# Kernel tuning notes

Measured on AMD Instinct MI355X. Metric: run time of the kernel, lower is better.

## Reference

```python
import jax, jax.numpy as jnp
import numpy as np

MAX_SEQLEN = 2048  # static max sequence length (flash varlen APIs take this as a host arg)


def setup_inputs() -> dict:
    key = jax.random.key(0)
    k1, k2, k3 = jax.random.split(key, 3)
    T, H, D = 8192, 8, 128
    B = 4
    q = jax.random.normal(k1, (T, H, D), dtype=jnp.float32)
    k = jax.random.normal(k2, (T, H, D), dtype=jnp.float32)
    v = jax.random.normal(k3, (T, H, D), dtype=jnp.float32)
    cu = (jnp.arange(B + 1, dtype=jnp.int32) * (T // B))  # [0,2048,4096,6144,8192]
    return {"q": q, "k": k, "v": v, "cu_seqlens_q": cu, "cu_seqlens_k": cu}


def reference(q, k, v, cu_seqlens_q, cu_seqlens_k):
    """Varlen (ragged) multi-head attention, non-causal (flash_attn varlen default).

    q,k,v: [T, H, D] packed over sequences; cu_seqlens: [B+1] boundaries.
    Gathers each sequence into a padded [B, S, H, D] layout, computes
    per-sequence softmax(q k^T / sqrt(D)) v with padding masked, then
    scatters back to packed [T, H, D].
    """
    T, H, D = q.shape
    B = cu_seqlens_q.shape[0] - 1
    S = MAX_SEQLEN
    scale = 1.0 / jnp.sqrt(jnp.asarray(D, q.dtype))

    pos = jnp.arange(S)
    q_start = cu_seqlens_q[:-1]
    k_start = cu_seqlens_k[:-1]
    q_len = jnp.diff(cu_seqlens_q)  # [B]
    k_len = jnp.diff(cu_seqlens_k)

    q_idx = jnp.clip(q_start[:, None] + pos[None, :], 0, T - 1)  # [B, S]
    k_idx = jnp.clip(k_start[:, None] + pos[None, :], 0, T - 1)
    q_valid = pos[None, :] < q_len[:, None]  # [B, S]
    k_valid = pos[None, :] < k_len[:, None]

    qb = q[q_idx]  # [B, S, H, D]
    kb = k[k_idx]
    vb = v[k_idx]

    scores = jnp.einsum('bqhd,bkhd->bhqk', qb, kb) * scale  # [B, H, S, S]
    neg = jnp.asarray(-1e30, scores.dtype)
    scores = jnp.where(k_valid[:, None, None, :], scores, neg)
    attn = jax.nn.softmax(scores, axis=-1)
    ob = jnp.einsum('bhqk,bkhd->bqhd', attn, vb)  # [B, S, H, D]

    # zero padded query rows, then scatter-add back to packed layout
    ob = jnp.where(q_valid[:, :, None, None], ob, 0.0)
    out = jnp.zeros_like(q).at[q_idx.reshape(-1)].add(ob.reshape(B * S, H, D))
    return out
```

## Files before the change

kernel.cpp:

```cpp
#include <hip/hip_runtime.h>
#include <hip/hip_bf16.h>
#include <stdint.h>

#define HH 8
#define DD 128
#define MAXSEQ 2048
#define QBLK 128

typedef float f32x16 __attribute__((ext_vector_type(16)));
typedef short s16x8 __attribute__((ext_vector_type(8)));

__device__ __forceinline__ unsigned short f2bf(float x) {
  union { float f; uint32_t u; } v; v.f = x;
  uint32_t u = v.u;
  return (unsigned short)((u + 0x7FFFu + ((u >> 16) & 1u)) >> 16);
}

__device__ __forceinline__ void gload_lds16(const unsigned short* g, unsigned short* l) {
  __builtin_amdgcn_global_load_lds((const __attribute__((address_space(1))) void*)g,
                                   (__attribute__((address_space(3))) void*)l, 16, 0, 0);
}

__global__ void zero_rows(const int* __restrict__ cuq, float* __restrict__ out, int T, int B) {
  const int t = blockIdx.x * blockDim.x + threadIdx.x;
  if (t >= T) return;
  bool covered = false;
  for (int b = 0; b < B; ++b) {
    const int s = cuq[b];
    const int len = min(cuq[b + 1] - s, MAXSEQ);
    if (t >= s && t < s + len) covered = true;
  }
  if (!covered) {
    float4* p = (float4*)(out + (size_t)t * HH * DD);
#pragma unroll 4
    for (int i = 0; i < HH * DD / 4; ++i) p[i] = float4{0.f, 0.f, 0.f, 0.f};
  }
}

__global__ void kvconv(const float* __restrict__ k, const float* __restrict__ v,
                       unsigned short* __restrict__ kb2, unsigned short* __restrict__ vb2, int T) {
  const int TBc = T >> 5;
  const int total = TBc * HH * 512;
  int u = blockIdx.x * blockDim.x + threadIdx.x;
  if (u < total) {
    const int lp = u & 63;
    const int key = lp & 31, hi = lp >> 5;
    int r = u >> 6;
    const int c = r & 7; r >>= 3;
    const int tb = r % TBc;
    const int h = r / TBc;
    const int t = tb * 32 + key;
    const int d = c * 16 + hi * 8;
    const float* src = k + ((size_t)t * HH + h) * DD + d;
    float4 a = *(const float4*)src;
    float4 cc = *(const float4*)(src + 4);
    union { unsigned short us[8]; uint4 q; } w;
    w.us[0] = f2bf(a.x); w.us[1] = f2bf(a.y); w.us[2] = f2bf(a.z); w.us[3] = f2bf(a.w);
    w.us[4] = f2bf(cc.x); w.us[5] = f2bf(cc.y); w.us[6] = f2bf(cc.z); w.us[7] = f2bf(cc.w);
    *(uint4*)(kb2 + (size_t)u * 8) = w.q;
  } else if ((u -= total) < total) {
    const int lo = u & 31;
    const int hi = (u >> 5) & 1;
    const int i = (u >> 6) & 7;
    const int dt = i & 3, ks2 = i >> 2;
    int r = u >> 9;
    const int tb = r % TBc;
    const int h = r / TBc;
    const int d = dt * 32 + lo;
    union { unsigned short us[8]; uint4 q; } w;
#pragma unroll
    for (int j = 0; j < 8; ++j) {
      const int phys = 16 * ks2 + ((j < 4) ? (4 * hi + j) : (8 + 4 * hi + (j - 4)));
      const int t = tb * 32 + phys;
      w.us[j] = f2bf(v[((size_t)t * HH + h) * DD + d]);
    }
    *(uint4*)(vb2 + (size_t)u * 8) = w.q;
  }
}

__global__ __launch_bounds__(256, 2)
void attn_main(const float* __restrict__ q,
               const unsigned short* __restrict__ kb2,
               const unsigned short* __restrict__ vb2,
               const int* __restrict__ cuq,
               const int* __restrict__ cuk,
               float* __restrict__ out,
               int T, int BH) {
  extern __shared__ __align__(16) unsigned short smem[];

  const int TBc = T >> 5;
  const int bid = blockIdx.x;
  const int bh = bid % BH;
  const int qt = bid / BH;
  const int b = bh / HH, h = bh % HH;
  const int qs = cuq[b], qe = cuq[b + 1];
  const int ks = cuk[b], ke = cuk[b + 1];
  const int nq = min(qe - qs, MAXSEQ);
  const int nk = min(ke - ks, MAXSEQ);
  if (qt * QBLK >= nq || nk <= 0) return;

  const int tid = threadIdx.x;
  const int wave = tid >> 6;
  const int lane = tid & 63;
  const int lo = lane & 31;
  const int hi = lane >> 5;
  const int wub = (tid & ~63) * 8;

  const int kb32 = ks >> 5;
  const unsigned short* kb2h = kb2 + (size_t)h * TBc * 4096;
  const unsigned short* vb2h = vb2 + (size_t)h * TBc * 4096;

  const float SC = (1.0f / 11.313708498984761f) * 1.4426950408889634f;
  const int qrow = qt * QBLK + wave * 32 + lo;
  const int qg = qs + min(qrow, nq - 1);
  const float* qp = q + ((size_t)qg * HH + h) * DD;
  s16x8 qf[8];
#pragma unroll
  for (int c = 0; c < 8; ++c) {
    const float* p0 = qp + c * 16 + hi * 8;
    float4 a = *(const float4*)(p0);
    float4 cc = *(const float4*)(p0 + 4);
    union { unsigned short us[8]; s16x8 v; } u;
    u.us[0] = f2bf(a.x * SC); u.us[1] = f2bf(a.y * SC);
    u.us[2] = f2bf(a.z * SC); u.us[3] = f2bf(a.w * SC);
    u.us[4] = f2bf(cc.x * SC); u.us[5] = f2bf(cc.y * SC);
    u.us[6] = f2bf(cc.z * SC); u.us[7] = f2bf(cc.w * SC);
    qf[c] = u.v;
  }

  f32x16 Oa[4];
#pragma unroll
  for (int i = 0; i < 4; ++i)
#pragma unroll
    for (int r = 0; r < 16; ++r) Oa[i][r] = 0.0f;

  float l_run = 0.0f;
  const int nkt = (nk + 63) / 64;

  auto stage = [&](int buf, int kt) {
    unsigned short* Kd = smem + buf * 8192;
    unsigned short* Vd = smem + 16384 + buf * 8192;
#pragma unroll
    for (int r = 0; r < 4; ++r) {
      const int u = r * 256 + tid;
      const int tb = min(kb32 + 2 * kt + (u >> 9), TBc - 1);
      gload_lds16(kb2h + (size_t)tb * 4096 + (size_t)(u & 511) * 8, Kd + (size_t)(r * 256) * 8 + wub);
    }
#pragma unroll
    for (int r = 0; r < 4; ++r) {
      const int u = r * 256 + tid;
      const int tb = min(kb32 + 2 * kt + (u >> 9), TBc - 1);
      gload_lds16(vb2h + (size_t)tb * 4096 + (size_t)(u & 511) * 8, Vd + (size_t)(r * 256) * 8 + wub);
    }
  };

  stage(0, 0);
  __syncthreads();

  int buf = 0;
  for (int kt = 0; kt < nkt; ++kt) {
    if (kt + 1 < nkt) stage(buf ^ 1, kt + 1);

    const unsigned short* Kb = smem + buf * 8192;
    const unsigned short* Vb = smem + 16384 + buf * 8192;

    f32x16 st0, st1;
#pragma unroll
    for (int r = 0; r < 16; ++r) { st0[r] = 0.0f; st1[r] = 0.0f; }
    {
      s16x8 kfA[8], kfB[8];
#pragma unroll
      for (int c = 0; c < 8; ++c) kfA[c] = *(const s16x8*)(Kb + c * 512 + lane * 8);
#pragma unroll
      for (int c = 0; c < 8; ++c) kfB[c] = *(const s16x8*)(Kb + 4096 + c * 512 + lane * 8);
      __builtin_amdgcn_s_setprio(1);
#pragma unroll
      for (int c = 0; c < 8; ++c) {
        st0 = __builtin_amdgcn_mfma_f32_32x32x16_bf16(kfA[c], qf[c], st0, 0, 0, 0);
        st1 = __builtin_amdgcn_mfma_f32_32x32x16_bf16(kfB[c], qf[c], st1, 0, 0, 0);
      }
      __builtin_amdgcn_s_setprio(0);
    }

    const int lim = nk - kt * 64;
    if (lim < 64) {
#pragma unroll
      for (int r = 0; r < 16; ++r) {
        const int a = (r & 3) + 8 * (r >> 2) + 4 * hi;
        if (a >= lim) st0[r] = -__builtin_inff();
        if (a + 32 >= lim) st1[r] = -__builtin_inff();
      }
    }

    float p[32];
#pragma unroll
    for (int r = 0; r < 16; ++r) {
      p[r] = __builtin_amdgcn_exp2f(st0[r]);
      p[16 + r] = __builtin_amdgcn_exp2f(st1[r]);
    }
    float ps = 0.f;
#pragma unroll
    for (int r = 0; r < 32; r += 4) ps += (p[r] + p[r + 1]) + (p[r + 2] + p[r + 3]);
    l_run += ps;

    uint32_t pw[16];
#pragma unroll
    for (int g = 0; g < 8; ++g) {
      uint32_t w0, w1;
      asm("v_cvt_pk_bf16_f32 %0, %1, %2" : "=v"(w0) : "v"(p[4 * g + 0]), "v"(p[4 * g + 1]));
      asm("v_cvt_pk_bf16_f32 %0, %1, %2" : "=v"(w1) : "v"(p[4 * g + 2]), "v"(p[4 * g + 3]));
      pw[2 * g] = w0;
      pw[2 * g + 1] = w1;
    }

    {
      s16x8 vf[16];
#pragma unroll
      for (int i = 0; i < 8; ++i) vf[i] = *(const s16x8*)(Vb + i * 512 + lane * 8);
#pragma unroll
      for (int i = 0; i < 8; ++i) vf[8 + i] = *(const s16x8*)(Vb + 4096 + i * 512 + lane * 8);
      __builtin_amdgcn_s_setprio(1);
#pragma unroll
      for (int Hk = 0; Hk < 4; ++Hk) {
        union { uint32_t u[4]; s16x8 v; } pa;
        pa.u[0] = pw[4 * Hk + 0]; pa.u[1] = pw[4 * Hk + 1];
        pa.u[2] = pw[4 * Hk + 2]; pa.u[3] = pw[4 * Hk + 3];
        const int H = Hk >> 1, ks2 = Hk & 1;
#pragma unroll
        for (int dt = 0; dt < 4; ++dt)
          Oa[dt] = __builtin_amdgcn_mfma_f32_32x32x16_bf16(pa.v, vf[H * 8 + ks2 * 4 + dt], Oa[dt], 0, 0, 0);
      }
      __builtin_amdgcn_s_setprio(0);
    }

    if (kt + 1 < nkt) {
      __syncthreads();
      buf ^= 1;
    }
  }

  l_run += __shfl_xor(l_run, 32);
  const float linv = 1.0f / l_run;
#pragma unroll
  for (int r = 0; r < 16; ++r) {
    const int src = (r & 3) + 8 * (r >> 2) + 4 * hi;
    const float li = __shfl(linv, src);
    const int qirow = qt * QBLK + wave * 32 + src;
    if (qirow < nq) {
      float* op = out + ((size_t)(qs + qirow) * HH + h) * DD;
      op[0 * 32 + lo] = Oa[0][r] * li;
      op[1 * 32 + lo] = Oa[1][r] * li;
      op[2 * 32 + lo] = Oa[2][r] * li;
      op[3 * 32 + lo] = Oa[3][r] * li;
    }
  }
}

extern "C" void kernel_launch(void* const* d_in, const int* in_sizes, int n_in,
                              void* d_out, int out_size, void* d_ws, size_t ws_size,
                              hipStream_t stream) {
  const float* q = (const float*)d_in[0];
  const float* k = (const float*)d_in[1];
  const float* v = (const float*)d_in[2];
  const int* cuq = (const int*)d_in[3];
  const int* cuk = (const int*)d_in[4];
  float* out = (float*)d_out;
  const int T = in_sizes[0] / (HH * DD);
  const int B = in_sizes[3] - 1;

  unsigned short* kb2 = (unsigned short*)d_ws;
  unsigned short* vb2 = kb2 + (size_t)T * HH * DD;
  const size_t need = (size_t)T * HH * DD * 2 * 2;
  if (ws_size < need) return;

  {
    zero_rows<<<(T + 255) / 256, 256, 0, stream>>>(cuq, out, T, B);
  }
  {
    const int total = (T >> 5) * HH * 512;
    kvconv<<<(2 * total + 255) / 256, 256, 0, stream>>>(k, v, kb2, vb2, T);
  }
  {
    const int BH = B * HH;
    const int scap = MAXSEQ < T ? MAXSEQ : T;
    const int qtiles = (scap + QBLK - 1) / QBLK;
    attn_main<<<BH * qtiles, 256, 65536, stream>>>(q, kb2, vb2, cuq, cuk, out, T, BH);
  }
}
```

Measured before the change: 104.1 us.

## Load V fragments directly from global into registers instead of LDS staging

V tiles are no longer staged through shared memory. Each wave now loads its V fragments straight from global memory into registers, one half before the QK^T MFMAs and the other half after them, so the latency overlaps with compute. Only K stays double-buffered in LDS, which cuts dynamic shared memory from 64KB to 32KB and may allow more blocks per CU. The cost is that every wave fetches the same V data from global/L2 separately, and register pressure goes up.

```diff
diff --git a/kernel.cpp b/kernel.cpp
--- a/kernel.cpp
+++ b/kernel.cpp
@@ -137,49 +137,61 @@
   float l_run = 0.0f;
   const int nkt = (nk + 63) / 64;
 
-  auto stage = [&](int buf, int kt) {
+  auto stageK = [&](int buf, int kt) {
     unsigned short* Kd = smem + buf * 8192;
-    unsigned short* Vd = smem + 16384 + buf * 8192;
 #pragma unroll
     for (int r = 0; r < 4; ++r) {
       const int u = r * 256 + tid;
       const int tb = min(kb32 + 2 * kt + (u >> 9), TBc - 1);
       gload_lds16(kb2h + (size_t)tb * 4096 + (size_t)(u & 511) * 8, Kd + (size_t)(r * 256) * 8 + wub);
     }
-#pragma unroll
-    for (int r = 0; r < 4; ++r) {
-      const int u = r * 256 + tid;
-      const int tb = min(kb32 + 2 * kt + (u >> 9), TBc - 1);
-      gload_lds16(vb2h + (size_t)tb * 4096 + (size_t)(u & 511) * 8, Vd + (size_t)(r * 256) * 8 + wub);
-    }
   };
 
-  stage(0, 0);
+  stageK(0, 0);
   __syncthreads();
 
   int buf = 0;
   for (int kt = 0; kt < nkt; ++kt) {
-    if (kt + 1 < nkt) stage(buf ^ 1, kt + 1);
+    s16x8 vfA[8];
+    {
+      const size_t base = (size_t)min(kb32 + 2 * kt, TBc - 1) * 4096;
+#pragma unroll
+      for (int i = 0; i < 8; ++i) vfA[i] = *(const s16x8*)(vb2h + base + i * 512 + lane * 8);
+    }
+
+    if (kt + 1 < nkt) stageK(buf ^ 1, kt + 1);
 
     const unsigned short* Kb = smem + buf * 8192;
-    const unsigned short* Vb = smem + 16384 + buf * 8192;
 
     f32x16 st0, st1;
 #pragma unroll
     for (int r = 0; r < 16; ++r) { st0[r] = 0.0f; st1[r] = 0.0f; }
     {
-      s16x8 kfA[8], kfB[8];
+      s16x8 kfA[8];
 #pragma unroll
       for (int c = 0; c < 8; ++c) kfA[c] = *(const s16x8*)(Kb + c * 512 + lane * 8);
+      __builtin_amdgcn_s_setprio(1);
+#pragma unroll
+      for (int c = 0; c < 8; ++c)
+        st0 = __builtin_amdgcn_mfma_f32_32x32x16_bf16(kfA[c], qf[c], st0, 0, 0, 0);
+      __builtin_amdgcn_s_setprio(0);
+    }
+    {
+      s16x8 kfB[8];
 #pragma unroll
       for (int c = 0; c < 8; ++c) kfB[c] = *(const s16x8*)(Kb + 4096 + c * 512 + lane * 8);
       __builtin_amdgcn_s_setprio(1);
 #pragma unroll
-      for (int c = 0; c < 8; ++c) {
-        st0 = __builtin_amdgcn_mfma_f32_32x32x16_bf16(kfA[c], qf[c], st0, 0, 0, 0);
+      for (int c = 0; c < 8; ++c)
         st1 = __builtin_amdgcn_mfma_f32_32x32x16_bf16(kfB[c], qf[c], st1, 0, 0, 0);
-      }
       __builtin_amdgcn_s_setprio(0);
+    }
+
+    s16x8 vfB[8];
+    {
+      const size_t base = (size_t)min(kb32 + 2 * kt + 1, TBc - 1) * 4096;
+#pragma unroll
+      for (int i = 0; i < 8; ++i) vfB[i] = *(const s16x8*)(vb2h + base + i * 512 + lane * 8);
     }
 
     const int lim = nk - kt * 64;
@@ -213,25 +225,26 @@
       pw[2 * g + 1] = w1;
     }
 
-    {
-      s16x8 vf[16];
-#pragma unroll
-      for (int i = 0; i < 8; ++i) vf[i] = *(const s16x8*)(Vb + i * 512 + lane * 8);
-#pragma unroll
-      for (int i = 0; i < 8; ++i) vf[8 + i] = *(const s16x8*)(Vb + 4096 + i * 512 + lane * 8);
-      __builtin_amdgcn_s_setprio(1);
-#pragma unroll
-      for (int Hk = 0; Hk < 4; ++Hk) {
-        union { uint32_t u[4]; s16x8 v; } pa;
-        pa.u[0] = pw[4 * Hk + 0]; pa.u[1] = pw[4 * Hk + 1];
-        pa.u[2] = pw[4 * Hk + 2]; pa.u[3] = pw[4 * Hk + 3];
-        const int H = Hk >> 1, ks2 = Hk & 1;
-#pragma unroll
-        for (int dt = 0; dt < 4; ++dt)
-          Oa[dt] = __builtin_amdgcn_mfma_f32_32x32x16_bf16(pa.v, vf[H * 8 + ks2 * 4 + dt], Oa[dt], 0, 0, 0);
-      }
-      __builtin_amdgcn_s_setprio(0);
-    }
+    __builtin_amdgcn_s_setprio(1);
+#pragma unroll
+    for (int ks2 = 0; ks2 < 2; ++ks2) {
+      union { uint32_t u[4]; s16x8 v; } pa;
+      pa.u[0] = pw[4 * ks2 + 0]; pa.u[1] = pw[4 * ks2 + 1];
+      pa.u[2] = pw[4 * ks2 + 2]; pa.u[3] = pw[4 * ks2 + 3];
+#pragma unroll
+      for (int dt = 0; dt < 4; ++dt)
+        Oa[dt] = __builtin_amdgcn_mfma_f32_32x32x16_bf16(pa.v, vfA[ks2 * 4 + dt], Oa[dt], 0, 0, 0);
+    }
+#pragma unroll
+    for (int ks2 = 0; ks2 < 2; ++ks2) {
+      union { uint32_t u[4]; s16x8 v; } pa;
+      pa.u[0] = pw[8 + 4 * ks2 + 0]; pa.u[1] = pw[8 + 4 * ks2 + 1];
+      pa.u[2] = pw[8 + 4 * ks2 + 2]; pa.u[3] = pw[8 + 4 * ks2 + 3];
+#pragma unroll
+      for (int dt = 0; dt < 4; ++dt)
+        Oa[dt] = __builtin_amdgcn_mfma_f32_32x32x16_bf16(pa.v, vfB[ks2 * 4 + dt], Oa[dt], 0, 0, 0);
+    }
+    __builtin_amdgcn_s_setprio(0);
 
     if (kt + 1 < nkt) {
       __syncthreads();
@@ -284,6 +297,6 @@
     const int BH = B * HH;
     const int scap = MAXSEQ < T ? MAXSEQ : T;
     const int qtiles = (scap + QBLK - 1) / QBLK;
-    attn_main<<<BH * qtiles, 256, 65536, stream>>>(q, kb2, vb2, cuq, cuk, out, T, BH);
-  }
-}
+    attn_main<<<BH * qtiles, 256, 32768, stream>>>(q, kb2, vb2, cuq, cuk, out, T, BH);
+  }
+}
```

After: 110.3 us. 6.0% more time.
